# Optimization experiments

Measured on AMD Instinct MI355X. Metric: run time of the kernel, lower is better.

The kernel has to match this reference:

```python
import jax, jax.numpy as jnp
import numpy as np

TOPK_CONF = 100   # cfg.nms_top_k_conf
TOPK_IOU = 15     # cfg.nms_top_k_iou
IOU_GAUSS = (32, 32)  # cfg.iou_gauss_dim
EPS = 1e-6        # cfg.positive


def unnormal_gaussian(mask_shape, loc):
    """loc: [..., 4] = (cx, cy, w, h) in [0,1). Returns [..., H, W] unnormalized gaussians."""
    H, W = mask_shape
    ys = (jnp.arange(H, dtype=loc.dtype) + 0.5) / H  # [H]
    xs = (jnp.arange(W, dtype=loc.dtype) + 0.5) / W  # [W]
    cx, cy = loc[..., 0], loc[..., 1]
    sx = jnp.abs(loc[..., 2]) * 0.5 + 1e-3
    sy = jnp.abs(loc[..., 3]) * 0.5 + 1e-3
    dx2 = (xs - cx[..., None]) ** 2 / (2.0 * sx[..., None] ** 2)  # [..., W]
    dy2 = (ys - cy[..., None]) ** 2 / (2.0 * sy[..., None] ** 2)  # [..., H]
    return jnp.exp(-(dy2[..., :, None] + dx2[..., None, :]))      # [..., H, W]


def setup_inputs() -> dict:
    key = jax.random.key(0)
    k1, k2, k3, k4, k5 = jax.random.split(key, 5)
    B, P, C, M = 4, 19248, 81, 32
    original = jax.random.normal(k1, (B, 3, 550, 550), dtype=jnp.float32)
    loc = jax.random.uniform(k2, (B, P, 4), dtype=jnp.float32)  # cx,cy,w,h in [0,1)
    conf = jax.random.normal(k3, (B, P, C), dtype=jnp.float32)
    mask = jax.random.normal(k4, (B, P, M), dtype=jnp.float32)
    proto = jax.random.normal(k5, (B, 138, 138, M), dtype=jnp.float32)
    return {"original": original, "loc": loc, "conf": conf, "mask": mask, "proto": proto}


def reference(original, loc, conf, mask, proto):
    B, H, W = original.shape[0], original.shape[2], original.shape[3]
    # class-1 foreground confidence after softmax over classes
    conf1 = jax.nn.softmax(conf, axis=2)[:, :, 1]  # [B, P]

    # ---- detect(): top-k by conf, pairwise gaussian IoU, keep lowest-overlap boxes ----
    order = jnp.argsort(-conf1, axis=-1)[:, :TOPK_CONF]                    # [B, K]
    sconf = jnp.take_along_axis(conf1, order, axis=1)                      # [B, K]
    sloc = jnp.take_along_axis(loc, order[..., None], axis=1)              # [B, K, 4]
    smask = jnp.take_along_axis(mask, order[..., None], axis=1)            # [B, K, Mdim]

    gauss = unnormal_gaussian(IOU_GAUSS, sloc)                             # [B, K, G, G]
    g_rows = gauss[:, None, :, :, :]                                       # broadcast [B,1,K,G,G]
    g_cols = gauss[:, :, None, :, :]                                       # broadcast [B,K,1,G,G]
    inter = jnp.sum(jnp.minimum(g_rows, g_cols), axis=(-2, -1))            # [B, K, K]
    union = jnp.sum(jnp.maximum(g_rows, g_cols), axis=(-2, -1))            # [B, K, K]
    gauss_iou = inter / union
    iou_max = jnp.max(jnp.triu(gauss_iou, k=1), axis=1)                    # [B, K]
    keep = jnp.argsort(iou_max, axis=-1)[:, :TOPK_IOU]                     # [B, Kk]

    kloc = jnp.take_along_axis(sloc, keep[..., None], axis=1)              # [B, Kk, 4]
    kmask = jnp.take_along_axis(smask, keep[..., None], axis=1)            # [B, Kk, Mdim]
    kconf = jnp.take_along_axis(sconf, keep, axis=1)                       # [B, Kk]

    # ---- VarianceLoss ----
    Hp, Wp = proto.shape[1], proto.shape[2]
    ug = unnormal_gaussian((Hp, Wp), kloc)                                 # [B, Kk, Hp, Wp]
    assembled = jax.nn.sigmoid(jnp.einsum('bhwm,bkm->bkhw', proto, kmask)) # lincomb + sigmoid
    attention = assembled * ug
    mask_conf = attention * kconf[:, :, None, None]                        # einsum('abcd,ab->abcd')
    denom = jnp.sum(mask_conf, axis=1, keepdims=True) + EPS
    final_conf = 1.0 - jnp.sum(mask_conf ** 2 / denom, axis=1)             # [B, Hp, Wp]
    final_conf = jnp.where(jnp.isnan(final_conf), 0.0, final_conf)

    resized = jax.image.resize(final_conf, (B, H, W), method='bilinear')   # [B, H, W]
    total_conf = jnp.sum(resized, axis=0)                                  # [H, W]
    weighted_mean = jnp.einsum('bchw,bhw->chw', original, resized)         # [C, H, W]
    squared_diff = (original - weighted_mean) ** 2
    weighted_diff = squared_diff * resized[:, None, :, :]                  # einsum('abcd,acd->abcd')
    weighted_var = weighted_diff / (total_conf + EPS)
    return jnp.sum(weighted_var) / 100.0
```

## Files before the change

kernel.cpp:

```cpp
#include <hip/hip_runtime.h>
#include <math.h>

#define B 4
#define P 19248
#define C 81
#define M 32
#define K1 100
#define K2 15
#define G 32
#define HP 138
#define HO 550
#define FEPS 1e-6f
#define NLOC 19

#define NBUCKET 8192
#define CAP 2048

#define TI 16
#define NT 7
#define NTP 28
#define CH 128
#define NCH 8
#define SP 132

__global__ void k_conf1(const float* __restrict__ conf, float* __restrict__ conf1) {
    int gid  = blockIdx.x * blockDim.x + threadIdx.x;
    int wave = gid >> 6;
    int lane = threadIdx.x & 63;
    if (wave >= B * P) return;
    const float* row = conf + (size_t)wave * C;
    float x0 = (lane < C)      ? row[lane]      : -INFINITY;
    float x1 = (lane + 64 < C) ? row[lane + 64] : -INFINITY;
    float m = fmaxf(x0, x1);
#pragma unroll
    for (int o = 32; o; o >>= 1) m = fmaxf(m, __shfl_xor(m, o, 64));
    float s = 0.f;
    if (lane < C)      s += expf(x0 - m);
    if (lane + 64 < C) s += expf(x1 - m);
#pragma unroll
    for (int o = 32; o; o >>= 1) s += __shfl_xor(s, o, 64);
    if (lane == 0) conf1[wave] = expf(row[1] - m) / s;
}

__global__ __launch_bounds__(1024) void k_top100(
    const float* __restrict__ conf1, const float* __restrict__ loc,
    const float* __restrict__ mask,  int* __restrict__ order,
    float* __restrict__ sconf, float* __restrict__ sloc,
    float* __restrict__ smask) {
    int b = blockIdx.x;
    int tid = threadIdx.x;
    const float* c1 = conf1 + (size_t)b * P;

    __shared__ unsigned int hist[NBUCKET];
    __shared__ unsigned int gsum_[1024];
    __shared__ unsigned int g2[64];
    __shared__ unsigned long long keys[CAP];
    __shared__ int s_T;
    __shared__ int s_cnt;
    __shared__ int   s_order[K1];
    __shared__ float s_conf[K1];

    for (int i = tid; i < NBUCKET; i += 1024) hist[i] = 0;
    if (tid == 0) s_cnt = 0;
    __syncthreads();

    unsigned int mybits[NLOC];
#pragma unroll
    for (int s = 0; s < NLOC; ++s) {
        int p = tid + s * 1024;
        mybits[s] = (p < P) ? __float_as_uint(c1[p]) : 0u;
        if (p < P) atomicAdd(&hist[mybits[s] >> 17], 1u);
    }
    __syncthreads();

    {
        unsigned int gs = 0;
#pragma unroll
        for (int i = 0; i < 8; ++i) gs += hist[tid * 8 + i];
        gsum_[tid] = gs;
    }
    __syncthreads();
    if (tid < 64) {
        unsigned int gs = 0;
#pragma unroll
        for (int i = 0; i < 16; ++i) gs += gsum_[tid * 16 + i];
        g2[tid] = gs;
    }
    __syncthreads();

    if (tid == 0) {
        int cum = 0;
        int S = 63;
        for (; S > 0; --S) {
            if (cum + (int)g2[S] >= K1) break;
            cum += (int)g2[S];
        }
        int gI = S * 16 + 15;
        for (; gI > S * 16; --gI) {
            if (cum + (int)gsum_[gI] >= K1) break;
            cum += (int)gsum_[gI];
        }
        int T = gI * 8 + 7;
        for (; T > gI * 8; --T) {
            cum += (int)hist[T];
            if (cum >= K1) break;
        }
        s_T = T;
    }
    __syncthreads();

    int T = s_T;
#pragma unroll
    for (int s = 0; s < NLOC; ++s) {
        int p = tid + s * 1024;
        if (p < P && (int)(mybits[s] >> 17) >= T) {
            int pos = atomicAdd(&s_cnt, 1);
            if (pos < CAP)
                keys[pos] = ((unsigned long long)mybits[s] << 32)
                          | (unsigned int)(0xFFFFFFFFu - (unsigned int)p);
        }
    }
    __syncthreads();
    int nc = min(s_cnt, CAP);

    if (tid < nc) {
        unsigned long long mk = keys[tid];
        int rank = 0;
        for (int i = 0; i < nc; ++i) rank += (keys[i] > mk);
        if (rank < K1) {
            unsigned int bits = (unsigned int)(mk >> 32);
            int idx = (int)(0xFFFFFFFFu - (unsigned int)(mk & 0xFFFFFFFFu));
            s_order[rank] = idx;
            s_conf[rank] = __uint_as_float(bits);
        }
    }
    __syncthreads();

    for (int t = tid; t < K1; t += 1024) {
        order[b * K1 + t] = s_order[t];
        sconf[b * K1 + t] = s_conf[t];
    }
    for (int t = tid; t < K1 * 4; t += 1024) {
        int k = t >> 2, d = t & 3;
        sloc[(b * K1 + k) * 4 + d] = loc[((size_t)b * P + s_order[k]) * 4 + d];
    }
    for (int t = tid; t < K1 * M; t += 1024) {
        int k = t >> 5, d = t & 31;
        smask[(b * K1 + k) * M + d] = mask[((size_t)b * P + s_order[k]) * M + d];
    }
}

__global__ void k_gauss(const float* __restrict__ sloc, float* __restrict__ gauss) {
    int bk = blockIdx.x;
    const float* l = sloc + bk * 4;
    float cx = l[0], cy = l[1];
    float sx = fabsf(l[2]) * 0.5f + 0.001f;
    float sy = fabsf(l[3]) * 0.5f + 0.001f;
    float dsx = 2.f * sx * sx;
    float dsy = 2.f * sy * sy;
    for (int p = threadIdx.x; p < G * G; p += 256) {
        int y = p >> 5, x = p & 31;
        float xs = (x + 0.5f) / (float)G;
        float ys = (y + 0.5f) / (float)G;
        float dx2 = (xs - cx) * (xs - cx) / dsx;
        float dy2 = (ys - cy) * (ys - cy) / dsy;
        gauss[(size_t)bk * (G * G) + p] = expf(-(dy2 + dx2));
    }
}

__global__ __launch_bounds__(256) void k_iou_tile(
    const float* __restrict__ gauss, float* __restrict__ Ibuf,
    float* __restrict__ Ubuf) {
    int ch = blockIdx.x;
    int tp = blockIdx.y;
    int b  = blockIdx.z;
    int ti = 0, rem = tp;
    while (rem >= NT - ti) { rem -= NT - ti; ++ti; }
    int tj = ti + rem;

    __shared__ __align__(16) float As[TI][SP];
    __shared__ __align__(16) float Bs[TI][SP];

    int tid = threadIdx.x;
    for (int idx = tid; idx < TI * (CH / 4); idx += 256) {
        int g = idx >> 5, v = idx & 31;
        int gi = ti * TI + g;
        float4 f = make_float4(0.f, 0.f, 0.f, 0.f);
        if (gi < K1)
            f = *(const float4*)(gauss + ((size_t)(b * K1 + gi) << 10) + ch * CH + v * 4);
        *(float4*)(&As[g][v * 4]) = f;
        int gj = tj * TI + g;
        float4 h = make_float4(0.f, 0.f, 0.f, 0.f);
        if (gj < K1)
            h = *(const float4*)(gauss + ((size_t)(b * K1 + gj) << 10) + ch * CH + v * 4);
        *(float4*)(&Bs[g][v * 4]) = h;
    }
    __syncthreads();

    int li = tid >> 4, lj = tid & 15;
    int i = ti * TI + li, j = tj * TI + lj;
    if (i < j && j < K1) {
        const float4* ar = (const float4*)(&As[li][0]);
        const float4* br = (const float4*)(&Bs[lj][0]);
        float inter = 0.f, uni = 0.f;
#pragma unroll
        for (int p = 0; p < CH / 4; ++p) {
            float4 a = ar[p], c = br[p];
            inter += fminf(a.x, c.x) + fminf(a.y, c.y)
                   + fminf(a.z, c.z) + fminf(a.w, c.w);
            uni   += fmaxf(a.x, c.x) + fmaxf(a.y, c.y)
                   + fmaxf(a.z, c.z) + fmaxf(a.w, c.w);
        }
        atomicAdd(&Ibuf[(b * K1 + i) * K1 + j], inter);
        atomicAdd(&Ubuf[(b * K1 + i) * K1 + j], uni);
    }
}

__global__ void k_combine(const float* __restrict__ Ibuf, const float* __restrict__ Ubuf,
                          unsigned int* __restrict__ ioumax) {
    int gid = blockIdx.x * 256 + threadIdx.x;
    if (gid >= B * K1 * K1) return;
    int b = gid / (K1 * K1);
    int rem = gid - b * K1 * K1;
    int i = rem / K1, j = rem % K1;
    if (i >= j) return;
    float iou = Ibuf[gid] / Ubuf[gid];
    atomicMax(&ioumax[b * K1 + j], __float_as_uint(iou));
}

__global__ void k_keep(const unsigned int* __restrict__ ioumax,
                       const float* __restrict__ sloc, const float* __restrict__ smask,
                       const float* __restrict__ sconf,
                       float* __restrict__ kloc, float* __restrict__ kmask,
                       float* __restrict__ kconf) {
    int b = blockIdx.x;
    int lane = threadIdx.x;
    float v0 = (lane < K1)      ? __uint_as_float(ioumax[b * K1 + lane])      : INFINITY;
    float v1 = (lane + 64 < K1) ? __uint_as_float(ioumax[b * K1 + lane + 64]) : INFINITY;
    __shared__ int s_keep[K2];
    for (int k = 0; k < K2; ++k) {
        float bv; int bi;
        if (v0 <= v1) { bv = v0; bi = lane; }
        else          { bv = v1; bi = lane + 64; }
#pragma unroll
        for (int o = 32; o; o >>= 1) {
            float ov = __shfl_xor(bv, o, 64);
            int   oi = __shfl_xor(bi, o, 64);
            if (ov < bv || (ov == bv && oi < bi)) { bv = ov; bi = oi; }
        }
        if (bi == lane)           v0 = INFINITY;
        else if (bi == lane + 64) v1 = INFINITY;
        if (lane == 0) s_keep[k] = bi;
    }
    __syncthreads();
    for (int t = lane; t < K2 * M; t += 64) {
        int k = t >> 5, d = t & 31;
        kmask[(b * K2 + k) * M + d] = smask[(b * K1 + s_keep[k]) * M + d];
    }
    for (int t = lane; t < K2 * 4; t += 64) {
        int k = t >> 2, d = t & 3;
        kloc[(b * K2 + k) * 4 + d] = sloc[(b * K1 + s_keep[k]) * 4 + d];
    }
    if (lane < K2) kconf[b * K2 + lane] = sconf[b * K1 + s_keep[lane]];
}

__global__ __launch_bounds__(256) void k_fconf(
    const float* __restrict__ proto, const float* __restrict__ kloc,
    const float* __restrict__ kmask, const float* __restrict__ kconf,
    float* __restrict__ fconf) {
    int b = blockIdx.y;
    int px0 = blockIdx.x * 256;
    int tid = threadIdx.x;
    __shared__ float s_pv[256][M + 1];
    __shared__ float s_km[K2][M];
    __shared__ float s_loc[K2][4];
    __shared__ float s_cf[K2];
    for (int t = tid; t < K2 * M; t += 256) s_km[t >> 5][t & 31] = kmask[b * K2 * M + t];
    for (int t = tid; t < K2 * 4; t += 256) s_loc[t >> 2][t & 3] = kloc[b * K2 * 4 + t];
    if (tid < K2) s_cf[tid] = kconf[b * K2 + tid];

    int nvalid = min(256, HP * HP - px0);
    const float4* pr4 = (const float4*)(proto + ((size_t)b * (HP * HP) + px0) * M);
    for (int idx = tid; idx < nvalid * (M / 4); idx += 256) {
        float4 f = pr4[idx];
        int q = idx >> 3, v = idx & 7;
        s_pv[q][v * 4 + 0] = f.x;
        s_pv[q][v * 4 + 1] = f.y;
        s_pv[q][v * 4 + 2] = f.z;
        s_pv[q][v * 4 + 3] = f.w;
    }
    __syncthreads();

    if (tid < nvalid) {
        int p = px0 + tid;
        int h = p / HP, w = p % HP;
        float pv[M];
#pragma unroll
        for (int m = 0; m < M; ++m) pv[m] = s_pv[tid][m];
        float ys = (h + 0.5f) / (float)HP;
        float xs = (w + 0.5f) / (float)HP;
        float sum_a = 0.f, sum_a2 = 0.f;
#pragma unroll 1
        for (int k = 0; k < K2; ++k) {
            float d = 0.f;
#pragma unroll
            for (int m = 0; m < M; ++m) d += pv[m] * s_km[k][m];
            float sig = 1.f / (1.f + expf(-d));
            float cx = s_loc[k][0], cy = s_loc[k][1];
            float sx = fabsf(s_loc[k][2]) * 0.5f + 0.001f;
            float sy = fabsf(s_loc[k][3]) * 0.5f + 0.001f;
            float dx2 = (xs - cx) * (xs - cx) / (2.f * sx * sx);
            float dy2 = (ys - cy) * (ys - cy) / (2.f * sy * sy);
            float ug = expf(-(dy2 + dx2));
            float a = sig * ug * s_cf[k];
            sum_a  += a;
            sum_a2 += a * a;
        }
        float fin = 1.f - sum_a2 / (sum_a + FEPS);
        if (!(fin == fin)) fin = 0.f;
        fconf[(size_t)b * HP * HP + p] = fin;
    }
}

__global__ void k_reduce(const float* __restrict__ fconf, const float* __restrict__ original,
                         float* __restrict__ acc) {
    int idx = blockIdx.x * 256 + threadIdx.x;
    float contrib = 0.f;
    if (idx < HO * HO) {
        int y = idx / HO, x = idx % HO;
        const float scale = (float)HP / (float)HO;
        float fy = (y + 0.5f) * scale - 0.5f;
        float fx = (x + 0.5f) * scale - 0.5f;
        float y0f = floorf(fy), x0f = floorf(fx);
        float wy = fy - y0f, wx = fx - x0f;
        int y0 = (int)y0f, x0 = (int)x0f;
        int iy0 = max(y0, 0), iy1 = min(y0 + 1, HP - 1);
        int ix0 = max(x0, 0), ix1 = min(x0 + 1, HP - 1);
        float r[B];
#pragma unroll
        for (int b = 0; b < B; ++b) {
            const float* F = fconf + (size_t)b * HP * HP;
            float v00 = F[iy0 * HP + ix0], v01 = F[iy0 * HP + ix1];
            float v10 = F[iy1 * HP + ix0], v11 = F[iy1 * HP + ix1];
            r[b] = (1.f - wy) * ((1.f - wx) * v00 + wx * v01)
                 +        wy  * ((1.f - wx) * v10 + wx * v11);
        }
        float t = r[0] + r[1] + r[2] + r[3];
        float s = 0.f;
#pragma unroll
        for (int c = 0; c < 3; ++c) {
            float o[B], wm = 0.f;
#pragma unroll
            for (int b = 0; b < B; ++b) {
                o[b] = original[(((size_t)b * 3 + c) * HO + y) * HO + x];
                wm += o[b] * r[b];
            }
#pragma unroll
            for (int b = 0; b < B; ++b) {
                float d = o[b] - wm;
                s += d * d * r[b];
            }
        }
        contrib = s / (t + FEPS);
    }
    __shared__ float red[256];
    red[threadIdx.x] = contrib;
    __syncthreads();
    for (int off = 128; off; off >>= 1) {
        if (threadIdx.x < off) red[threadIdx.x] += red[threadIdx.x + off];
        __syncthreads();
    }
    if (threadIdx.x == 0) atomicAdd(acc, red[0]);
}

__global__ void k_final(const float* __restrict__ acc, float* __restrict__ out) {
    out[0] = acc[0] / 100.f;
}

extern "C" void kernel_launch(void* const* d_in, const int* in_sizes, int n_in,
                              void* d_out, int out_size, void* d_ws, size_t ws_size,
                              hipStream_t stream) {
    (void)in_sizes; (void)n_in; (void)out_size; (void)ws_size;
    const float* original = (const float*)d_in[0];
    const float* loc      = (const float*)d_in[1];
    const float* conf     = (const float*)d_in[2];
    const float* mask     = (const float*)d_in[3];
    const float* proto    = (const float*)d_in[4];

    char* ws = (char*)d_ws;
    size_t off = 0;
    auto alloc = [&](size_t bytes) -> void* {
        void* p = ws + off;
        off += (bytes + 255) & ~(size_t)255;
        return p;
    };
    float* conf1        = (float*)alloc((size_t)B * P * sizeof(float));
    int*   order        = (int*)  alloc((size_t)B * K1 * sizeof(int));
    float* sconf        = (float*)alloc((size_t)B * K1 * sizeof(float));
    float* sloc         = (float*)alloc((size_t)B * K1 * 4 * sizeof(float));
    float* smask        = (float*)alloc((size_t)B * K1 * M * sizeof(float));
    float* gauss        = (float*)alloc((size_t)B * K1 * G * G * sizeof(float));
    float* Ibuf         = (float*)alloc((size_t)B * K1 * K1 * sizeof(float));
    float* Ubuf         = (float*)alloc((size_t)B * K1 * K1 * sizeof(float));
    unsigned int* iomax = (unsigned int*)alloc((size_t)B * K1 * sizeof(unsigned int));
    float* kloc         = (float*)alloc((size_t)B * K2 * 4 * sizeof(float));
    float* kmask        = (float*)alloc((size_t)B * K2 * M * sizeof(float));
    float* kconf        = (float*)alloc((size_t)B * K2 * sizeof(float));
    float* fconf        = (float*)alloc((size_t)B * HP * HP * sizeof(float));
    float* acc          = (float*)alloc(sizeof(float));

    hipMemsetAsync(iomax, 0, (size_t)B * K1 * sizeof(unsigned int), stream);
    hipMemsetAsync(Ibuf, 0, (size_t)B * K1 * K1 * sizeof(float) * 2, stream);
    hipMemsetAsync(Ubuf, 0, (size_t)B * K1 * K1 * sizeof(float), stream);
    hipMemsetAsync(acc, 0, sizeof(float), stream);

    k_conf1<<<(B * P) / 4, 256, 0, stream>>>(conf, conf1);
    k_top100<<<B, 1024, 0, stream>>>(conf1, loc, mask, order, sconf, sloc, smask);
    k_gauss<<<B * K1, 256, 0, stream>>>(sloc, gauss);
    dim3 g4(NCH, NTP, B);
    k_iou_tile<<<g4, 256, 0, stream>>>(gauss, Ibuf, Ubuf);
    k_combine<<<(B * K1 * K1 + 255) / 256, 256, 0, stream>>>(Ibuf, Ubuf, iomax);
    k_keep<<<B, 64, 0, stream>>>(iomax, sloc, smask, sconf, kloc, kmask, kconf);
    dim3 g6((HP * HP + 255) / 256, B);
    k_fconf<<<g6, 256, 0, stream>>>(proto, kloc, kmask, kconf, fconf);
    k_reduce<<<(HO * HO + 255) / 256, 256, 0, stream>>>(fconf, original, acc);
    k_final<<<1, 1, 0, stream>>>(acc, (float*)d_out);
}
```

Measured before the change: 179.3 us.

## Fold memsets and small kernels into neighbours, loop IoU chunks in-block

Removes the four hipMemsetAsync calls by zeroing ioumax and the output inside k_gauss. Replaces the chunk-split IoU kernel plus atomic I/U buffers and the separate combine kernel with one kernel that loops over all chunks in-block and does the atomicMax directly. Drops the final divide kernel by scaling in k_reduce's atomicAdd and drops the unused order output. The goal is fewer launches and fewer global atomics, at the cost of fewer blocks (less parallelism) in the IoU stage.

```diff
diff --git a/kernel.cpp b/kernel.cpp
--- a/kernel.cpp
+++ b/kernel.cpp
@@ -44,7 +44,7 @@
 
 __global__ __launch_bounds__(1024) void k_top100(
     const float* __restrict__ conf1, const float* __restrict__ loc,
-    const float* __restrict__ mask,  int* __restrict__ order,
+    const float* __restrict__ mask,
     float* __restrict__ sconf, float* __restrict__ sloc,
     float* __restrict__ smask) {
     int b = blockIdx.x;
@@ -137,7 +137,6 @@
     __syncthreads();
 
     for (int t = tid; t < K1; t += 1024) {
-        order[b * K1 + t] = s_order[t];
         sconf[b * K1 + t] = s_conf[t];
     }
     for (int t = tid; t < K1 * 4; t += 1024) {
@@ -150,8 +149,11 @@
     }
 }
 
-__global__ void k_gauss(const float* __restrict__ sloc, float* __restrict__ gauss) {
+__global__ void k_gauss(const float* __restrict__ sloc, float* __restrict__ gauss,
+                        unsigned int* __restrict__ ioumax, float* __restrict__ out) {
     int bk = blockIdx.x;
+    if (threadIdx.x == 0) ioumax[bk] = 0u;
+    if (bk == 0 && threadIdx.x == 1) out[0] = 0.f;
     const float* l = sloc + bk * 4;
     float cx = l[0], cy = l[1];
     float sx = fabsf(l[2]) * 0.5f + 0.001f;
@@ -168,12 +170,10 @@
     }
 }
 
-__global__ __launch_bounds__(256) void k_iou_tile(
-    const float* __restrict__ gauss, float* __restrict__ Ibuf,
-    float* __restrict__ Ubuf) {
-    int ch = blockIdx.x;
-    int tp = blockIdx.y;
-    int b  = blockIdx.z;
+__global__ __launch_bounds__(256) void k_iou(
+    const float* __restrict__ gauss, unsigned int* __restrict__ ioumax) {
+    int tp = blockIdx.x;
+    int b  = blockIdx.y;
     int ti = 0, rem = tp;
     while (rem >= NT - ti) { rem -= NT - ti; ++ti; }
     int tj = ti + rem;
@@ -182,27 +182,28 @@
     __shared__ __align__(16) float Bs[TI][SP];
 
     int tid = threadIdx.x;
-    for (int idx = tid; idx < TI * (CH / 4); idx += 256) {
-        int g = idx >> 5, v = idx & 31;
-        int gi = ti * TI + g;
-        float4 f = make_float4(0.f, 0.f, 0.f, 0.f);
-        if (gi < K1)
-            f = *(const float4*)(gauss + ((size_t)(b * K1 + gi) << 10) + ch * CH + v * 4);
-        *(float4*)(&As[g][v * 4]) = f;
-        int gj = tj * TI + g;
-        float4 h = make_float4(0.f, 0.f, 0.f, 0.f);
-        if (gj < K1)
-            h = *(const float4*)(gauss + ((size_t)(b * K1 + gj) << 10) + ch * CH + v * 4);
-        *(float4*)(&Bs[g][v * 4]) = h;
-    }
-    __syncthreads();
-
     int li = tid >> 4, lj = tid & 15;
     int i = ti * TI + li, j = tj * TI + lj;
-    if (i < j && j < K1) {
+
+    float inter = 0.f, uni = 0.f;
+    for (int ch = 0; ch < NCH; ++ch) {
+        __syncthreads();
+        for (int idx = tid; idx < TI * (CH / 4); idx += 256) {
+            int g = idx >> 5, v = idx & 31;
+            int gi = ti * TI + g;
+            float4 f = make_float4(0.f, 0.f, 0.f, 0.f);
+            if (gi < K1)
+                f = *(const float4*)(gauss + ((size_t)(b * K1 + gi) << 10) + ch * CH + v * 4);
+            *(float4*)(&As[g][v * 4]) = f;
+            int gj = tj * TI + g;
+            float4 h = make_float4(0.f, 0.f, 0.f, 0.f);
+            if (gj < K1)
+                h = *(const float4*)(gauss + ((size_t)(b * K1 + gj) << 10) + ch * CH + v * 4);
+            *(float4*)(&Bs[g][v * 4]) = h;
+        }
+        __syncthreads();
         const float4* ar = (const float4*)(&As[li][0]);
         const float4* br = (const float4*)(&Bs[lj][0]);
-        float inter = 0.f, uni = 0.f;
 #pragma unroll
         for (int p = 0; p < CH / 4; ++p) {
             float4 a = ar[p], c = br[p];
@@ -211,21 +212,11 @@
             uni   += fmaxf(a.x, c.x) + fmaxf(a.y, c.y)
                    + fmaxf(a.z, c.z) + fmaxf(a.w, c.w);
         }
-        atomicAdd(&Ibuf[(b * K1 + i) * K1 + j], inter);
-        atomicAdd(&Ubuf[(b * K1 + i) * K1 + j], uni);
-    }
-}
-
-__global__ void k_combine(const float* __restrict__ Ibuf, const float* __restrict__ Ubuf,
-                          unsigned int* __restrict__ ioumax) {
-    int gid = blockIdx.x * 256 + threadIdx.x;
-    if (gid >= B * K1 * K1) return;
-    int b = gid / (K1 * K1);
-    int rem = gid - b * K1 * K1;
-    int i = rem / K1, j = rem % K1;
-    if (i >= j) return;
-    float iou = Ibuf[gid] / Ubuf[gid];
-    atomicMax(&ioumax[b * K1 + j], __float_as_uint(iou));
+    }
+    if (i < j && j < K1) {
+        float iou = inter / uni;
+        atomicMax(&ioumax[b * K1 + j], __float_as_uint(iou));
+    }
 }
 
 __global__ void k_keep(const unsigned int* __restrict__ ioumax,
@@ -323,7 +314,7 @@
 }
 
 __global__ void k_reduce(const float* __restrict__ fconf, const float* __restrict__ original,
-                         float* __restrict__ acc) {
+                         float* __restrict__ out) {
     int idx = blockIdx.x * 256 + threadIdx.x;
     float contrib = 0.f;
     if (idx < HO * HO) {
@@ -370,11 +361,7 @@
         if (threadIdx.x < off) red[threadIdx.x] += red[threadIdx.x + off];
         __syncthreads();
     }
-    if (threadIdx.x == 0) atomicAdd(acc, red[0]);
-}
-
-__global__ void k_final(const float* __restrict__ acc, float* __restrict__ out) {
-    out[0] = acc[0] / 100.f;
+    if (threadIdx.x == 0) atomicAdd(out, red[0] * 0.01f);
 }
 
 extern "C" void kernel_launch(void* const* d_in, const int* in_sizes, int n_in,
@@ -386,6 +373,7 @@
     const float* conf     = (const float*)d_in[2];
     const float* mask     = (const float*)d_in[3];
     const float* proto    = (const float*)d_in[4];
+    float* out = (float*)d_out;
 
     char* ws = (char*)d_ws;
     size_t off = 0;
@@ -395,34 +383,23 @@
         return p;
     };
     float* conf1        = (float*)alloc((size_t)B * P * sizeof(float));
-    int*   order        = (int*)  alloc((size_t)B * K1 * sizeof(int));
     float* sconf        = (float*)alloc((size_t)B * K1 * sizeof(float));
     float* sloc         = (float*)alloc((size_t)B * K1 * 4 * sizeof(float));
     float* smask        = (float*)alloc((size_t)B * K1 * M * sizeof(float));
     float* gauss        = (float*)alloc((size_t)B * K1 * G * G * sizeof(float));
-    float* Ibuf         = (float*)alloc((size_t)B * K1 * K1 * sizeof(float));
-    float* Ubuf         = (float*)alloc((size_t)B * K1 * K1 * sizeof(float));
     unsigned int* iomax = (unsigned int*)alloc((size_t)B * K1 * sizeof(unsigned int));
     float* kloc         = (float*)alloc((size_t)B * K2 * 4 * sizeof(float));
     float* kmask        = (float*)alloc((size_t)B * K2 * M * sizeof(float));
     float* kconf        = (float*)alloc((size_t)B * K2 * sizeof(float));
     float* fconf        = (float*)alloc((size_t)B * HP * HP * sizeof(float));
-    float* acc          = (float*)alloc(sizeof(float));
-
-    hipMemsetAsync(iomax, 0, (size_t)B * K1 * sizeof(unsigned int), stream);
-    hipMemsetAsync(Ibuf, 0, (size_t)B * K1 * K1 * sizeof(float) * 2, stream);
-    hipMemsetAsync(Ubuf, 0, (size_t)B * K1 * K1 * sizeof(float), stream);
-    hipMemsetAsync(acc, 0, sizeof(float), stream);
 
     k_conf1<<<(B * P) / 4, 256, 0, stream>>>(conf, conf1);
-    k_top100<<<B, 1024, 0, stream>>>(conf1, loc, mask, order, sconf, sloc, smask);
-    k_gauss<<<B * K1, 256, 0, stream>>>(sloc, gauss);
-    dim3 g4(NCH, NTP, B);
-    k_iou_tile<<<g4, 256, 0, stream>>>(gauss, Ibuf, Ubuf);
-    k_combine<<<(B * K1 * K1 + 255) / 256, 256, 0, stream>>>(Ibuf, Ubuf, iomax);
+    k_top100<<<B, 1024, 0, stream>>>(conf1, loc, mask, sconf, sloc, smask);
+    k_gauss<<<B * K1, 256, 0, stream>>>(sloc, gauss, iomax, out);
+    dim3 g4(NTP, B);
+    k_iou<<<g4, 256, 0, stream>>>(gauss, iomax);
     k_keep<<<B, 64, 0, stream>>>(iomax, sloc, smask, sconf, kloc, kmask, kconf);
     dim3 g6((HP * HP + 255) / 256, B);
     k_fconf<<<g6, 256, 0, stream>>>(proto, kloc, kmask, kconf, fconf);
-    k_reduce<<<(HO * HO + 255) / 256, 256, 0, stream>>>(fconf, original, acc);
-    k_final<<<1, 1, 0, stream>>>(acc, (float*)d_out);
-}
+    k_reduce<<<(HO * HO + 255) / 256, 256, 0, stream>>>(fconf, original, out);
+}
```

Result: slower. 188.0 us (+4.8%).
